# Performance work log

Measured on AMD Instinct MI355X. Metric: run time of the kernel, lower is better.

Reference implementation:

```python
import jax, jax.numpy as jnp
import numpy as np

NUM_NODES = 10000
NUM_EDGES = 640000
D_FEAT = 128

def setup_inputs() -> dict:
    key = jax.random.key(0)
    k1, k2 = jax.random.split(key)
    x = jax.random.normal(k1, (NUM_NODES, D_FEAT), dtype=jnp.float32)
    edge_index = jax.random.randint(k2, (2, NUM_EDGES), 0, NUM_NODES, dtype=jnp.int64)
    return {"x": x, "edge_index": edge_index}

def reference(x, edge_index):
    # MessagePassing(aggr='add') with default message/update:
    # msg = x[src]; out[n] = sum of msg over edges with dst == n
    src, dst = edge_index[0], edge_index[1]
    msg = x[src]                                   # [num_edges, d]
    out = jax.ops.segment_sum(msg, dst, num_segments=NUM_NODES)  # [num_nodes, d]
    return out
```

## Files before the change

kernel.cpp:

```cpp
#include <hip/hip_runtime.h>

#define NUM_NODES 10000
#define NUM_EDGES 640000
#define D_FEAT 128

#define BSHIFT 4
#define NPB 16
#define NB 625
#define BLOCKS 256
#define EPB (NUM_EDGES / BLOCKS)
#define CELL_CAP 32
#define MAXB 1344

#define XB_U4 (NUM_NODES * 16)
#define CVT_PER_BLOCK (XB_U4 / BLOCKS)


__device__ __forceinline__ unsigned bf16_rne(float f) {
    unsigned u = __float_as_uint(f);
    return (u + 0x7FFFu + ((u >> 16) & 1u)) >> 16;
}

__global__ __launch_bounds__(1024) void scatter_cvt_kernel(
    const int* __restrict__ ei, const float4* __restrict__ x4,
    uint4* __restrict__ xb, unsigned* __restrict__ cnt,
    unsigned* __restrict__ slots) {
    __shared__ int cur[NB];
    int t = threadIdx.x, b = blockIdx.x;
    if (t < NB) cur[t] = 0;

    if (t < CVT_PER_BLOCK) {
        int o = b * CVT_PER_BLOCK + t;
        float4 a = x4[2 * o];
        float4 c = x4[2 * o + 1];
        uint4 w;
        w.x = bf16_rne(a.x) | (bf16_rne(a.y) << 16);
        w.y = bf16_rne(a.z) | (bf16_rne(a.w) << 16);
        w.z = bf16_rne(c.x) | (bf16_rne(c.y) << 16);
        w.w = bf16_rne(c.z) | (bf16_rne(c.w) << 16);
        xb[o] = w;
    }

    int base = b * EPB;
    int s0 = ei[base + t];
    int d0 = ei[NUM_EDGES + base + t];
    int s1 = ei[base + t + 1024];
    int d1 = ei[NUM_EDGES + base + t + 1024];
    int s2 = 0, d2 = 0;
    bool has2 = (t + 2048) < EPB;
    if (has2) {
        s2 = ei[base + t + 2048];
        d2 = ei[NUM_EDGES + base + t + 2048];
    }
    __syncthreads();

    {
        int k = d0 >> BSHIFT;
        int pos = atomicAdd(&cur[k], 1);
        if (pos < CELL_CAP)
            slots[(unsigned)(k * BLOCKS + b) * CELL_CAP + (unsigned)pos] =
                ((unsigned)(d0 & (NPB - 1)) << 16) | (unsigned)s0;
    }
    {
        int k = d1 >> BSHIFT;
        int pos = atomicAdd(&cur[k], 1);
        if (pos < CELL_CAP)
            slots[(unsigned)(k * BLOCKS + b) * CELL_CAP + (unsigned)pos] =
                ((unsigned)(d1 & (NPB - 1)) << 16) | (unsigned)s1;
    }
    if (has2) {
        int k = d2 >> BSHIFT;
        int pos = atomicAdd(&cur[k], 1);
        if (pos < CELL_CAP)
            slots[(unsigned)(k * BLOCKS + b) * CELL_CAP + (unsigned)pos] =
                ((unsigned)(d2 & (NPB - 1)) << 16) | (unsigned)s2;
    }
    __syncthreads();
    if (t < NB) cnt[b * NB + t] = (unsigned)min(cur[t], CELL_CAP);
}

__device__ __forceinline__ void acc8(float* a, uint4 w) {
    a[0] += __uint_as_float(w.x << 16);
    a[1] += __uint_as_float(w.x & 0xFFFF0000u);
    a[2] += __uint_as_float(w.y << 16);
    a[3] += __uint_as_float(w.y & 0xFFFF0000u);
    a[4] += __uint_as_float(w.z << 16);
    a[5] += __uint_as_float(w.z & 0xFFFF0000u);
    a[6] += __uint_as_float(w.w << 16);
    a[7] += __uint_as_float(w.w & 0xFFFF0000u);
}

__device__ __forceinline__ void reduce_write(float* a, int node, int q, int sub,
                                             float4* __restrict__ out4) {
    #pragma unroll
    for (int r = 0; r < 8; ++r) {
        a[r] += __shfl_down(a[r], 32);
        a[r] += __shfl_down(a[r], 16);
    }
    if (q == 0) {
        unsigned o = (unsigned)node * 32u + (unsigned)sub * 2u;
        out4[o]     = make_float4(a[0], a[1], a[2], a[3]);
        out4[o + 1] = make_float4(a[4], a[5], a[6], a[7]);
    }
}

__global__ __launch_bounds__(512) void sort_gather_kernel(
    const uint4* __restrict__ xb,
    const unsigned* __restrict__ cnt,
    const uint4* __restrict__ slots4,
    float4* __restrict__ out4)
{
    __shared__ int s_cnt[BLOCKS];
    __shared__ unsigned s_src[MAXB];
    __shared__ int h[NPB];
    __shared__ int off16[NPB];
    __shared__ int cur16[NPB];

    int k = blockIdx.x;
    int t = threadIdx.x;

    if (t < NPB) h[t] = 0;
    if (t < BLOCKS) s_cnt[t] = (int)cnt[t * NB + k];
    __syncthreads();

    const uint4* sb = slots4 + (unsigned)k * BLOCKS * (CELL_CAP / 4);
    uint4 w4[4];
    int vc[4];
    #pragma unroll
    for (int i = 0; i < 4; ++i) {
        int c = (t >> 3) + 64 * i;
        int sub = t & 7;
        w4[i] = sb[t + 512 * i];
        int v = s_cnt[c] - sub * 4;
        vc[i] = max(0, min(4, v));
        if (vc[i] > 0) atomicAdd(&h[w4[i].x >> 16], 1);
        if (vc[i] > 1) atomicAdd(&h[w4[i].y >> 16], 1);
        if (vc[i] > 2) atomicAdd(&h[w4[i].z >> 16], 1);
        if (vc[i] > 3) atomicAdd(&h[w4[i].w >> 16], 1);
    }
    __syncthreads();

    if (t < NPB) {
        int v = h[t];
        int s = v;
        #pragma unroll
        for (int d = 1; d < 16; d <<= 1) {
            int u = __shfl_up(s, d, 16);
            if (t >= d) s += u;
        }
        off16[t] = s - v;
        cur16[t] = s - v;
    }
    __syncthreads();

    #pragma unroll
    for (int i = 0; i < 4; ++i) {
        if (vc[i] > 0) { int p = atomicAdd(&cur16[w4[i].x >> 16], 1); if (p < MAXB) s_src[p] = w4[i].x & 0xFFFFu; }
        if (vc[i] > 1) { int p = atomicAdd(&cur16[w4[i].y >> 16], 1); if (p < MAXB) s_src[p] = w4[i].y & 0xFFFFu; }
        if (vc[i] > 2) { int p = atomicAdd(&cur16[w4[i].z >> 16], 1); if (p < MAXB) s_src[p] = w4[i].z & 0xFFFFu; }
        if (vc[i] > 3) { int p = atomicAdd(&cur16[w4[i].w >> 16], 1); if (p < MAXB) s_src[p] = w4[i].w & 0xFFFFu; }
    }
    __syncthreads();

    int wave = t >> 6;
    int lane = t & 63;
    int q    = lane >> 4;
    int sub  = lane & 15;

    int mA = wave;
    int mB = wave + 8;
    int begA = off16[mA], ecA = h[mA];
    int begB = off16[mB], ecB = h[mB];
    int lastA = ecA > 0 ? ecA - 1 : 0;
    int lastB = ecB > 0 ? ecB - 1 : 0;

    float aA[8] = {0.f, 0.f, 0.f, 0.f, 0.f, 0.f, 0.f, 0.f};
    float aB[8] = {0.f, 0.f, 0.f, 0.f, 0.f, 0.f, 0.f, 0.f};

    bool vA = q < ecA, vB = q < ecB;
    unsigned iA = (unsigned)min(begA + min(q, lastA), MAXB - 1);
    unsigned iB = (unsigned)min(begB + min(q, lastB), MAXB - 1);
    uint4 wA = xb[(s_src[iA] & 0xFFFFu) * 16u + (unsigned)sub];
    uint4 wB = xb[(s_src[iB] & 0xFFFFu) * 16u + (unsigned)sub];

    int jmax = max(ecA, ecB);
    for (int j = 0; j < jmax; j += 4) {
        int jn = j + 4;
        unsigned iA2 = (unsigned)min(begA + min(jn + q, lastA), MAXB - 1);
        unsigned iB2 = (unsigned)min(begB + min(jn + q, lastB), MAXB - 1);
        uint4 wA2 = xb[(s_src[iA2] & 0xFFFFu) * 16u + (unsigned)sub];
        uint4 wB2 = xb[(s_src[iB2] & 0xFFFFu) * 16u + (unsigned)sub];
        bool vA2 = (jn + q) < ecA;
        bool vB2 = (jn + q) < ecB;
        if (vA) acc8(aA, wA);
        if (vB) acc8(aB, wB);
        wA = wA2; vA = vA2;
        wB = wB2; vB = vB2;
    }

    reduce_write(aA, k * NPB + mA, q, sub, out4);
    reduce_write(aB, k * NPB + mB, q, sub, out4);
}

extern "C" void kernel_launch(void* const* d_in, const int* in_sizes, int n_in,
                              void* d_out, int out_size, void* d_ws, size_t ws_size,
                              hipStream_t stream) {
    const float* x   = (const float*)d_in[0];
    const int*   ei  = (const int*)d_in[1];
    float*       out = (float*)d_out;

    uint4*    xb    = (uint4*)d_ws;
    unsigned* cnt   = (unsigned*)(xb + XB_U4);
    unsigned* slots = cnt + BLOCKS * NB;

    scatter_cvt_kernel<<<BLOCKS, 1024, 0, stream>>>(
        ei, (const float4*)x, xb, cnt, slots);

    sort_gather_kernel<<<NB, 512, 0, stream>>>(
        xb, cnt, (const uint4*)slots, (float4*)out);
}
```

Before: 85.01 us.

## Replace per-block cell buckets with global atomic per-bucket segments

The scatter kernel now appends each edge directly into one contiguous per-bucket segment using global atomic counters, replacing the per-block LDS-counted cells. The gather kernel therefore reads a dense segment of up to 1344 entries instead of 256 sparse cells with per-cell counts, which cuts slot memory traffic and removes the cnt array. In exchange it adds a memset launch and heavy global atomic contention on 625 counters, plus atomicExch stores. It also relies on the random-input bound that no bucket exceeds 1344 edges.

After: 272.7 us. 221% more time.

```diff
diff --git a/kernel.cpp b/kernel.cpp
--- a/kernel.cpp
+++ b/kernel.cpp
@@ -7,13 +7,12 @@
 #define BSHIFT 4
 #define NPB 16
 #define NB 625
-#define BLOCKS 256
-#define EPB (NUM_EDGES / BLOCKS)
-#define CELL_CAP 32
-#define MAXB 1344
+#define SEG_CAP 1344
+#define MAXB SEG_CAP
 
 #define XB_U4 (NUM_NODES * 16)
-#define CVT_PER_BLOCK (XB_U4 / BLOCKS)
+
+#define K1_THREADS 1024
 
 
 __device__ __forceinline__ unsigned bf16_rne(float f) {
@@ -21,16 +20,18 @@
     return (u + 0x7FFFu + ((u >> 16) & 1u)) >> 16;
 }
 
-__global__ __launch_bounds__(1024) void scatter_cvt_kernel(
+__global__ __launch_bounds__(K1_THREADS) void scatter_kernel(
     const int* __restrict__ ei, const float4* __restrict__ x4,
-    uint4* __restrict__ xb, unsigned* __restrict__ cnt,
-    unsigned* __restrict__ slots) {
-    __shared__ int cur[NB];
+    uint4* __restrict__ xb, unsigned* __restrict__ gcur,
+    unsigned* __restrict__ seg)
+{
     int t = threadIdx.x, b = blockIdx.x;
-    if (t < NB) cur[t] = 0;
+    int idx = b * K1_THREADS + t;
+    int s = ei[idx];
+    int d = ei[NUM_EDGES + idx];
 
-    if (t < CVT_PER_BLOCK) {
-        int o = b * CVT_PER_BLOCK + t;
+    if (t < 256) {
+        int o = b * 256 + t;
         float4 a = x4[2 * o];
         float4 c = x4[2 * o + 1];
         uint4 w;
@@ -41,42 +42,11 @@
         xb[o] = w;
     }
 
-    int base = b * EPB;
-    int s0 = ei[base + t];
-    int d0 = ei[NUM_EDGES + base + t];
-    int s1 = ei[base + t + 1024];
-    int d1 = ei[NUM_EDGES + base + t + 1024];
-    int s2 = 0, d2 = 0;
-    bool has2 = (t + 2048) < EPB;
-    if (has2) {
-        s2 = ei[base + t + 2048];
-        d2 = ei[NUM_EDGES + base + t + 2048];
-    }
-    __syncthreads();
-
-    {
-        int k = d0 >> BSHIFT;
-        int pos = atomicAdd(&cur[k], 1);
-        if (pos < CELL_CAP)
-            slots[(unsigned)(k * BLOCKS + b) * CELL_CAP + (unsigned)pos] =
-                ((unsigned)(d0 & (NPB - 1)) << 16) | (unsigned)s0;
-    }
-    {
-        int k = d1 >> BSHIFT;
-        int pos = atomicAdd(&cur[k], 1);
-        if (pos < CELL_CAP)
-            slots[(unsigned)(k * BLOCKS + b) * CELL_CAP + (unsigned)pos] =
-                ((unsigned)(d1 & (NPB - 1)) << 16) | (unsigned)s1;
-    }
-    if (has2) {
-        int k = d2 >> BSHIFT;
-        int pos = atomicAdd(&cur[k], 1);
-        if (pos < CELL_CAP)
-            slots[(unsigned)(k * BLOCKS + b) * CELL_CAP + (unsigned)pos] =
-                ((unsigned)(d2 & (NPB - 1)) << 16) | (unsigned)s2;
-    }
-    __syncthreads();
-    if (t < NB) cnt[b * NB + t] = (unsigned)min(cur[t], CELL_CAP);
+    int k = d >> BSHIFT;
+    unsigned pos = atomicAdd(&gcur[k], 1u);
+    if (pos < SEG_CAP)
+        atomicExch(&seg[(unsigned)k * SEG_CAP + pos],
+                   ((unsigned)(d & (NPB - 1)) << 16) | (unsigned)s);
 }
 
 __device__ __forceinline__ void acc8(float* a, uint4 w) {
@@ -104,13 +74,12 @@
     }
 }
 
-__global__ __launch_bounds__(512) void sort_gather_kernel(
+__global__ __launch_bounds__(512) void gather_kernel(
     const uint4* __restrict__ xb,
-    const unsigned* __restrict__ cnt,
-    const uint4* __restrict__ slots4,
+    const unsigned* __restrict__ gcur,
+    const unsigned* __restrict__ seg,
     float4* __restrict__ out4)
 {
-    __shared__ int s_cnt[BLOCKS];
     __shared__ unsigned s_src[MAXB];
     __shared__ int h[NPB];
     __shared__ int off16[NPB];
@@ -120,24 +89,15 @@
     int t = threadIdx.x;
 
     if (t < NPB) h[t] = 0;
-    if (t < BLOCKS) s_cnt[t] = (int)cnt[t * NB + k];
+    int n = (int)min(gcur[k], (unsigned)SEG_CAP);
     __syncthreads();
 
-    const uint4* sb = slots4 + (unsigned)k * BLOCKS * (CELL_CAP / 4);
-    uint4 w4[4];
-    int vc[4];
-    #pragma unroll
-    for (int i = 0; i < 4; ++i) {
-        int c = (t >> 3) + 64 * i;
-        int sub = t & 7;
-        w4[i] = sb[t + 512 * i];
-        int v = s_cnt[c] - sub * 4;
-        vc[i] = max(0, min(4, v));
-        if (vc[i] > 0) atomicAdd(&h[w4[i].x >> 16], 1);
-        if (vc[i] > 1) atomicAdd(&h[w4[i].y >> 16], 1);
-        if (vc[i] > 2) atomicAdd(&h[w4[i].z >> 16], 1);
-        if (vc[i] > 3) atomicAdd(&h[w4[i].w >> 16], 1);
-    }
+    const unsigned* sg = seg + (unsigned)k * SEG_CAP;
+    unsigned e0 = 0, e1 = 0, e2 = 0;
+    bool v0 = t < n, v1 = t + 512 < n, v2 = t + 1024 < n;
+    if (v0) { e0 = sg[t];        atomicAdd(&h[e0 >> 16], 1); }
+    if (v1) { e1 = sg[t + 512];  atomicAdd(&h[e1 >> 16], 1); }
+    if (v2) { e2 = sg[t + 1024]; atomicAdd(&h[e2 >> 16], 1); }
     __syncthreads();
 
     if (t < NPB) {
@@ -153,13 +113,9 @@
     }
     __syncthreads();
 
-    #pragma unroll
-    for (int i = 0; i < 4; ++i) {
-        if (vc[i] > 0) { int p = atomicAdd(&cur16[w4[i].x >> 16], 1); if (p < MAXB) s_src[p] = w4[i].x & 0xFFFFu; }
-        if (vc[i] > 1) { int p = atomicAdd(&cur16[w4[i].y >> 16], 1); if (p < MAXB) s_src[p] = w4[i].y & 0xFFFFu; }
-        if (vc[i] > 2) { int p = atomicAdd(&cur16[w4[i].z >> 16], 1); if (p < MAXB) s_src[p] = w4[i].z & 0xFFFFu; }
-        if (vc[i] > 3) { int p = atomicAdd(&cur16[w4[i].w >> 16], 1); if (p < MAXB) s_src[p] = w4[i].w & 0xFFFFu; }
-    }
+    if (v0) { int p = atomicAdd(&cur16[e0 >> 16], 1); if (p < MAXB) s_src[p] = e0 & 0xFFFFu; }
+    if (v1) { int p = atomicAdd(&cur16[e1 >> 16], 1); if (p < MAXB) s_src[p] = e1 & 0xFFFFu; }
+    if (v2) { int p = atomicAdd(&cur16[e2 >> 16], 1); if (p < MAXB) s_src[p] = e2 & 0xFFFFu; }
     __syncthreads();
 
     int wave = t >> 6;
@@ -209,13 +165,15 @@
     const int*   ei  = (const int*)d_in[1];
     float*       out = (float*)d_out;
 
-    uint4*    xb    = (uint4*)d_ws;
-    unsigned* cnt   = (unsigned*)(xb + XB_U4);
-    unsigned* slots = cnt + BLOCKS * NB;
+    uint4*    xb   = (uint4*)d_ws;
+    unsigned* gcur = (unsigned*)(xb + XB_U4);
+    unsigned* seg  = gcur + 640;
 
-    scatter_cvt_kernel<<<BLOCKS, 1024, 0, stream>>>(
-        ei, (const float4*)x, xb, cnt, slots);
+    hipMemsetAsync(gcur, 0, NB * sizeof(unsigned), stream);
 
-    sort_gather_kernel<<<NB, 512, 0, stream>>>(
-        xb, cnt, (const uint4*)slots, (float4*)out);
+    scatter_kernel<<<NB, K1_THREADS, 0, stream>>>(
+        ei, (const float4*)x, xb, gcur, seg);
+
+    gather_kernel<<<NB, 512, 0, stream>>>(
+        xb, gcur, seg, (float4*)out);
 }
```

## Halve bucket cell capacity with global overflow list and one node per wave

Applied to the files above, without the earlier changes.

Cuts the per-cell slot capacity from 32 to 16, which halves the slot buffer written by the scatter kernel and read by the gather kernel. Edges that no longer fit go to a small global overflow list, and every gather block scans that list. The gather kernel now runs 1024 threads with one destination node per wave instead of two. Edge index loads are issued before the bf16 conversion so their latency overlaps it. The costs are an extra memset launch, a global atomic on every overflowing edge, and an overflow scan in all 625 blocks. Edges past the overflow cap would be dropped.

New measurement: 84.68 us. About the same (-0.4%).

```diff
diff --git a/kernel.cpp b/kernel.cpp
--- a/kernel.cpp
+++ b/kernel.cpp
@@ -9,8 +9,9 @@
 #define NB 625
 #define BLOCKS 256
 #define EPB (NUM_EDGES / BLOCKS)
-#define CELL_CAP 32
+#define CELL_CAP 16
 #define MAXB 1344
+#define OVF_CAP 1024
 
 #define XB_U4 (NUM_NODES * 16)
 #define CVT_PER_BLOCK (XB_U4 / BLOCKS)
@@ -24,10 +25,24 @@
 __global__ __launch_bounds__(1024) void scatter_cvt_kernel(
     const int* __restrict__ ei, const float4* __restrict__ x4,
     uint4* __restrict__ xb, unsigned* __restrict__ cnt,
-    unsigned* __restrict__ slots) {
+    unsigned* __restrict__ slots, unsigned* __restrict__ ovf_cnt,
+    unsigned* __restrict__ ovf)
+{
     __shared__ int cur[NB];
     int t = threadIdx.x, b = blockIdx.x;
     if (t < NB) cur[t] = 0;
+
+    int base = b * EPB;
+    int s0 = ei[base + t];
+    int d0 = ei[NUM_EDGES + base + t];
+    int s1 = ei[base + t + 1024];
+    int d1 = ei[NUM_EDGES + base + t + 1024];
+    int s2 = 0, d2 = 0;
+    bool has2 = (t + 2048) < EPB;
+    if (has2) {
+        s2 = ei[base + t + 2048];
+        d2 = ei[NUM_EDGES + base + t + 2048];
+    }
 
     if (t < CVT_PER_BLOCK) {
         int o = b * CVT_PER_BLOCK + t;
@@ -40,18 +55,6 @@
         w.w = bf16_rne(c.z) | (bf16_rne(c.w) << 16);
         xb[o] = w;
     }
-
-    int base = b * EPB;
-    int s0 = ei[base + t];
-    int d0 = ei[NUM_EDGES + base + t];
-    int s1 = ei[base + t + 1024];
-    int d1 = ei[NUM_EDGES + base + t + 1024];
-    int s2 = 0, d2 = 0;
-    bool has2 = (t + 2048) < EPB;
-    if (has2) {
-        s2 = ei[base + t + 2048];
-        d2 = ei[NUM_EDGES + base + t + 2048];
-    }
     __syncthreads();
 
     {
@@ -60,6 +63,12 @@
         if (pos < CELL_CAP)
             slots[(unsigned)(k * BLOCKS + b) * CELL_CAP + (unsigned)pos] =
                 ((unsigned)(d0 & (NPB - 1)) << 16) | (unsigned)s0;
+        else {
+            unsigned g = atomicAdd(ovf_cnt, 1u);
+            if (g < OVF_CAP)
+                ovf[g] = ((unsigned)k << 18) |
+                         ((unsigned)(d0 & (NPB - 1)) << 14) | (unsigned)s0;
+        }
     }
     {
         int k = d1 >> BSHIFT;
@@ -67,6 +76,12 @@
         if (pos < CELL_CAP)
             slots[(unsigned)(k * BLOCKS + b) * CELL_CAP + (unsigned)pos] =
                 ((unsigned)(d1 & (NPB - 1)) << 16) | (unsigned)s1;
+        else {
+            unsigned g = atomicAdd(ovf_cnt, 1u);
+            if (g < OVF_CAP)
+                ovf[g] = ((unsigned)k << 18) |
+                         ((unsigned)(d1 & (NPB - 1)) << 14) | (unsigned)s1;
+        }
     }
     if (has2) {
         int k = d2 >> BSHIFT;
@@ -74,6 +89,12 @@
         if (pos < CELL_CAP)
             slots[(unsigned)(k * BLOCKS + b) * CELL_CAP + (unsigned)pos] =
                 ((unsigned)(d2 & (NPB - 1)) << 16) | (unsigned)s2;
+        else {
+            unsigned g = atomicAdd(ovf_cnt, 1u);
+            if (g < OVF_CAP)
+                ovf[g] = ((unsigned)k << 18) |
+                         ((unsigned)(d2 & (NPB - 1)) << 14) | (unsigned)s2;
+        }
     }
     __syncthreads();
     if (t < NB) cnt[b * NB + t] = (unsigned)min(cur[t], CELL_CAP);
@@ -90,24 +111,12 @@
     a[7] += __uint_as_float(w.w & 0xFFFF0000u);
 }
 
-__device__ __forceinline__ void reduce_write(float* a, int node, int q, int sub,
-                                             float4* __restrict__ out4) {
-    #pragma unroll
-    for (int r = 0; r < 8; ++r) {
-        a[r] += __shfl_down(a[r], 32);
-        a[r] += __shfl_down(a[r], 16);
-    }
-    if (q == 0) {
-        unsigned o = (unsigned)node * 32u + (unsigned)sub * 2u;
-        out4[o]     = make_float4(a[0], a[1], a[2], a[3]);
-        out4[o + 1] = make_float4(a[4], a[5], a[6], a[7]);
-    }
-}
-
-__global__ __launch_bounds__(512) void sort_gather_kernel(
+__global__ __launch_bounds__(1024) void sort_gather_kernel(
     const uint4* __restrict__ xb,
     const unsigned* __restrict__ cnt,
     const uint4* __restrict__ slots4,
+    const unsigned* __restrict__ ovf_cnt,
+    const unsigned* __restrict__ ovf,
     float4* __restrict__ out4)
 {
     __shared__ int s_cnt[BLOCKS];
@@ -124,82 +133,79 @@
     __syncthreads();
 
     const uint4* sb = slots4 + (unsigned)k * BLOCKS * (CELL_CAP / 4);
-    uint4 w4[4];
-    int vc[4];
-    #pragma unroll
-    for (int i = 0; i < 4; ++i) {
-        int c = (t >> 3) + 64 * i;
-        int sub = t & 7;
-        w4[i] = sb[t + 512 * i];
-        int v = s_cnt[c] - sub * 4;
-        vc[i] = max(0, min(4, v));
-        if (vc[i] > 0) atomicAdd(&h[w4[i].x >> 16], 1);
-        if (vc[i] > 1) atomicAdd(&h[w4[i].y >> 16], 1);
-        if (vc[i] > 2) atomicAdd(&h[w4[i].z >> 16], 1);
-        if (vc[i] > 3) atomicAdd(&h[w4[i].w >> 16], 1);
+    uint4 w4 = sb[t];
+    int v = s_cnt[t >> 2] - (t & 3) * 4;
+    int vc = max(0, min(4, v));
+    if (vc > 0) atomicAdd(&h[w4.x >> 16], 1);
+    if (vc > 1) atomicAdd(&h[w4.y >> 16], 1);
+    if (vc > 2) atomicAdd(&h[w4.z >> 16], 1);
+    if (vc > 3) atomicAdd(&h[w4.w >> 16], 1);
+    int no = (int)min(*ovf_cnt, (unsigned)OVF_CAP);
+    for (int i = t; i < no; i += 1024) {
+        unsigned e = ovf[i];
+        if ((int)(e >> 18) == k) atomicAdd(&h[(e >> 14) & 15u], 1);
     }
     __syncthreads();
 
     if (t < NPB) {
-        int v = h[t];
-        int s = v;
+        int vv = h[t];
+        int s = vv;
         #pragma unroll
         for (int d = 1; d < 16; d <<= 1) {
             int u = __shfl_up(s, d, 16);
             if (t >= d) s += u;
         }
-        off16[t] = s - v;
-        cur16[t] = s - v;
-    }
-    __syncthreads();
-
-    #pragma unroll
-    for (int i = 0; i < 4; ++i) {
-        if (vc[i] > 0) { int p = atomicAdd(&cur16[w4[i].x >> 16], 1); if (p < MAXB) s_src[p] = w4[i].x & 0xFFFFu; }
-        if (vc[i] > 1) { int p = atomicAdd(&cur16[w4[i].y >> 16], 1); if (p < MAXB) s_src[p] = w4[i].y & 0xFFFFu; }
-        if (vc[i] > 2) { int p = atomicAdd(&cur16[w4[i].z >> 16], 1); if (p < MAXB) s_src[p] = w4[i].z & 0xFFFFu; }
-        if (vc[i] > 3) { int p = atomicAdd(&cur16[w4[i].w >> 16], 1); if (p < MAXB) s_src[p] = w4[i].w & 0xFFFFu; }
-    }
-    __syncthreads();
-
-    int wave = t >> 6;
+        off16[t] = s - vv;
+        cur16[t] = s - vv;
+    }
+    __syncthreads();
+
+    if (vc > 0) { int p = atomicAdd(&cur16[w4.x >> 16], 1); if (p < MAXB) s_src[p] = w4.x & 0xFFFFu; }
+    if (vc > 1) { int p = atomicAdd(&cur16[w4.y >> 16], 1); if (p < MAXB) s_src[p] = w4.y & 0xFFFFu; }
+    if (vc > 2) { int p = atomicAdd(&cur16[w4.z >> 16], 1); if (p < MAXB) s_src[p] = w4.z & 0xFFFFu; }
+    if (vc > 3) { int p = atomicAdd(&cur16[w4.w >> 16], 1); if (p < MAXB) s_src[p] = w4.w & 0xFFFFu; }
+    for (int i = t; i < no; i += 1024) {
+        unsigned e = ovf[i];
+        if ((int)(e >> 18) == k) {
+            int p = atomicAdd(&cur16[(e >> 14) & 15u], 1);
+            if (p < MAXB) s_src[p] = e & 0x3FFFu;
+        }
+    }
+    __syncthreads();
+
+    int m    = t >> 6;
     int lane = t & 63;
     int q    = lane >> 4;
     int sub  = lane & 15;
 
-    int mA = wave;
-    int mB = wave + 8;
-    int begA = off16[mA], ecA = h[mA];
-    int begB = off16[mB], ecB = h[mB];
-    int lastA = ecA > 0 ? ecA - 1 : 0;
-    int lastB = ecB > 0 ? ecB - 1 : 0;
-
-    float aA[8] = {0.f, 0.f, 0.f, 0.f, 0.f, 0.f, 0.f, 0.f};
-    float aB[8] = {0.f, 0.f, 0.f, 0.f, 0.f, 0.f, 0.f, 0.f};
-
-    bool vA = q < ecA, vB = q < ecB;
-    unsigned iA = (unsigned)min(begA + min(q, lastA), MAXB - 1);
-    unsigned iB = (unsigned)min(begB + min(q, lastB), MAXB - 1);
-    uint4 wA = xb[(s_src[iA] & 0xFFFFu) * 16u + (unsigned)sub];
-    uint4 wB = xb[(s_src[iB] & 0xFFFFu) * 16u + (unsigned)sub];
-
-    int jmax = max(ecA, ecB);
-    for (int j = 0; j < jmax; j += 4) {
+    int beg  = off16[m], ec = h[m];
+    int last = ec > 0 ? ec - 1 : 0;
+
+    float a[8] = {0.f, 0.f, 0.f, 0.f, 0.f, 0.f, 0.f, 0.f};
+
+    bool val = q < ec;
+    unsigned i0 = (unsigned)min(beg + min(q, last), MAXB - 1);
+    uint4 wv = xb[(s_src[i0] & 0xFFFFu) * 16u + (unsigned)sub];
+
+    for (int j = 0; j < ec; j += 4) {
         int jn = j + 4;
-        unsigned iA2 = (unsigned)min(begA + min(jn + q, lastA), MAXB - 1);
-        unsigned iB2 = (unsigned)min(begB + min(jn + q, lastB), MAXB - 1);
-        uint4 wA2 = xb[(s_src[iA2] & 0xFFFFu) * 16u + (unsigned)sub];
-        uint4 wB2 = xb[(s_src[iB2] & 0xFFFFu) * 16u + (unsigned)sub];
-        bool vA2 = (jn + q) < ecA;
-        bool vB2 = (jn + q) < ecB;
-        if (vA) acc8(aA, wA);
-        if (vB) acc8(aB, wB);
-        wA = wA2; vA = vA2;
-        wB = wB2; vB = vB2;
-    }
-
-    reduce_write(aA, k * NPB + mA, q, sub, out4);
-    reduce_write(aB, k * NPB + mB, q, sub, out4);
+        unsigned i1 = (unsigned)min(beg + min(jn + q, last), MAXB - 1);
+        uint4 wv1 = xb[(s_src[i1] & 0xFFFFu) * 16u + (unsigned)sub];
+        bool val1 = (jn + q) < ec;
+        if (val) acc8(a, wv);
+        wv = wv1; val = val1;
+    }
+
+    #pragma unroll
+    for (int r = 0; r < 8; ++r) {
+        a[r] += __shfl_down(a[r], 32);
+        a[r] += __shfl_down(a[r], 16);
+    }
+    if (q == 0) {
+        unsigned o = (unsigned)(k * NPB + m) * 32u + (unsigned)sub * 2u;
+        out4[o]     = make_float4(a[0], a[1], a[2], a[3]);
+        out4[o + 1] = make_float4(a[4], a[5], a[6], a[7]);
+    }
 }
 
 extern "C" void kernel_launch(void* const* d_in, const int* in_sizes, int n_in,
@@ -209,13 +215,17 @@
     const int*   ei  = (const int*)d_in[1];
     float*       out = (float*)d_out;
 
-    uint4*    xb    = (uint4*)d_ws;
-    unsigned* cnt   = (unsigned*)(xb + XB_U4);
-    unsigned* slots = cnt + BLOCKS * NB;
+    uint4*    xb      = (uint4*)d_ws;
+    unsigned* cnt     = (unsigned*)(xb + XB_U4);
+    unsigned* slots   = cnt + BLOCKS * NB;
+    unsigned* ovf_cnt = slots + (size_t)NB * BLOCKS * CELL_CAP;
+    unsigned* ovf     = ovf_cnt + 16;
+
+    hipMemsetAsync(ovf_cnt, 0, sizeof(unsigned), stream);
 
     scatter_cvt_kernel<<<BLOCKS, 1024, 0, stream>>>(
-        ei, (const float4*)x, xb, cnt, slots);
-
-    sort_gather_kernel<<<NB, 512, 0, stream>>>(
-        xb, cnt, (const uint4*)slots, (float4*)out);
-}
+        ei, (const float4*)x, xb, cnt, slots, ovf_cnt, ovf);
+
+    sort_gather_kernel<<<NB, 1024, 0, stream>>>(
+        xb, cnt, (const uint4*)slots, ovf_cnt, ovf, (float4*)out);
+}
```
